# Kernel tuning notes

Hardware: AMD Instinct MI355X
Metric: run time of the kernel (lower is better)

Reference implementation:

```python
import jax, jax.numpy as jnp
import numpy as np

R_SPHERE = 1.0   # conf['object_bounding_sphere']
N_STEPS = 64     # conf['n_steps']
N_IMPORT = 32    # forward default num_samples
VARI = 0.3       # forward default vari -> inv_s = exp(3)


def sdf_fn(pts):
    # analytic stand-in for implicit_network(x, expression)[..., 0]: sphere of radius 0.5
    return jnp.linalg.norm(pts, axis=-1) - 0.5


def sample_pdf(bins, weights, n_samples):
    # deterministic (det=True) CDF inversion, faithful to sample_pdf()
    weights = weights + 1e-8
    pdf = weights / jnp.sum(weights, -1, keepdims=True)
    cdf = jnp.cumsum(pdf, -1)
    cdf = jnp.concatenate([jnp.zeros_like(cdf[..., :1]), cdf], -1)  # [R, n]
    u = jnp.linspace(0.5 / n_samples, 1.0 - 0.5 / n_samples, n_samples, dtype=bins.dtype)
    u = jnp.broadcast_to(u, cdf.shape[:-1] + (n_samples,))          # [R, ns]
    inds = jax.vmap(lambda c, uu: jnp.searchsorted(c, uu, side='right'))(cdf, u)
    below = jnp.maximum(inds - 1, 0)
    above = jnp.minimum(inds, cdf.shape[-1] - 1)
    cdf_b = jnp.take_along_axis(cdf, below, -1)
    cdf_a = jnp.take_along_axis(cdf, above, -1)
    bins_b = jnp.take_along_axis(bins, below, -1)
    bins_a = jnp.take_along_axis(bins, above, -1)
    denom = cdf_a - cdf_b
    denom = jnp.where(denom < 1e-8, jnp.ones_like(denom), denom)
    t = (u - cdf_b) / denom
    return bins_b + t * (bins_a - bins_b)


def setup_inputs() -> dict:
    key = jax.random.key(0)
    k1, k2 = jax.random.split(key)
    rd = jax.random.normal(k1, (1, 262144, 3), dtype=jnp.float32)
    rd = rd / jnp.linalg.norm(rd, axis=-1, keepdims=True)  # unit ray directions
    cam_loc = jnp.array([[0.0, 0.0, 2.5]], dtype=jnp.float32)  # outside bounding sphere
    t_rand = jax.random.uniform(k2, (262144, N_STEPS), dtype=jnp.float32)
    return {"ray_dirs": rd, "cam_loc": cam_loc, "t_rand": t_rand}


def reference(ray_dirs, cam_loc, t_rand):
    b, p, _ = ray_dirs.shape
    # --- get_sphere_intersection ---
    ray_cam_dot = jnp.einsum('bpd,bd->bp', ray_dirs, cam_loc)              # [b,p]
    under = ray_cam_dot ** 2 - (jnp.sum(cam_loc ** 2, -1, keepdims=True) - R_SPHERE ** 2)
    under = under.reshape(-1)
    mask = under > 0
    sq = jnp.sqrt(jnp.where(mask, under, 0.0))
    si = sq[:, None] * jnp.array([-1.0, 1.0], dtype=ray_dirs.dtype) - ray_cam_dot.reshape(-1)[:, None]
    n_hit = jnp.maximum(jnp.sum(mask), 1)
    mean_si = jnp.sum(jnp.where(mask[:, None], si, 0.0), 0) / n_hit
    si = jnp.where(mask[:, None], si, mean_si[None, :])
    si = jnp.clip(si, 0.0, None)                                           # [b*p, 2]
    min_d, max_d = si[:, 0], si[:, 1]
    # --- eval_sdf_inside_sphere: stratified uniform samples (mask_intersect == all ones) ---
    steps = jnp.linspace(0.0, 1.0, N_STEPS, dtype=ray_dirs.dtype)[None, :]
    steps = steps * (max_d - min_d)[:, None] + min_d[:, None]
    sample_dist = ((max_d - min_d) / N_STEPS)[:, None]
    steps = steps + (t_rand - 0.5) * sample_dist                           # [R, n]
    origins = jnp.broadcast_to(cam_loc[:, None, :], (b, p, 3)).reshape(-1, 3)
    dirs = ray_dirs.reshape(-1, 3)
    pts = origins[:, None, :] + steps[..., None] * dirs[:, None, :]        # [R, n, 3]
    sdf = sdf_fn(pts)                                                      # [R, n]
    # --- NeuS alpha / weights ---
    inv_s = jnp.exp(jnp.asarray(VARI, ray_dirs.dtype) * 10.0)
    prev_cdf = jax.nn.sigmoid(sdf[:, :-1] * inv_s)
    next_cdf = jax.nn.sigmoid(sdf[:, 1:] * inv_s)
    alpha = jnp.clip((prev_cdf - next_cdf + 1e-8) / (prev_cdf + 1e-8), 0.0, 1.0)
    trans = jnp.cumprod(jnp.concatenate([jnp.ones((alpha.shape[0], 1), alpha.dtype),
                                         1.0 - alpha + 1e-7], -1), -1)[:, :-1]
    weights = alpha * trans                                                # [R, n-1]
    # --- up_sample: PDF importance resampling (searchsorted + gather) ---
    z_samples = sample_pdf(steps, weights, N_IMPORT)                       # [R, ns]
    new_samples = origins[:, None, :] + z_samples[..., None] * dirs[:, None, :]  # [R, ns, 3]
    return new_samples, z_samples, weights
```

## Files before the change

kernel.cpp:

```cpp
#include <hip/hip_runtime.h>


static constexpr int NSTEPS = 64;
static constexpr int NIMP   = 32;

template<int CTRL, int RM>
__device__ __forceinline__ float upd_dpp_f(float old, float src){
  return __int_as_float(__builtin_amdgcn_update_dpp(
      __float_as_int(old), __float_as_int(src), CTRL, RM, 0xF, false));
}

__device__ __forceinline__ float mul_scan64(float x){
  x *= upd_dpp_f<0x111,0xF>(1.0f, x);
  x *= upd_dpp_f<0x112,0xF>(1.0f, x);
  x *= upd_dpp_f<0x114,0xF>(1.0f, x);
  x *= upd_dpp_f<0x118,0xF>(1.0f, x);
  x *= upd_dpp_f<0x142,0xa>(1.0f, x);
  x *= upd_dpp_f<0x143,0xc>(1.0f, x);
  return x;
}
__device__ __forceinline__ float add_scan64(float x){
  x += upd_dpp_f<0x111,0xF>(0.0f, x);
  x += upd_dpp_f<0x112,0xF>(0.0f, x);
  x += upd_dpp_f<0x114,0xF>(0.0f, x);
  x += upd_dpp_f<0x118,0xF>(0.0f, x);
  x += upd_dpp_f<0x142,0xa>(0.0f, x);
  x += upd_dpp_f<0x143,0xc>(0.0f, x);
  return x;
}

__global__ __launch_bounds__(256) void si_partial_kernel(
    const float* __restrict__ rd, const float* __restrict__ cam,
    float* __restrict__ partial, int P)
{
  float cx = cam[0], cy = cam[1], cz = cam[2];
  float c2m = cx*cx + cy*cy + cz*cz - 1.0f;
  float s0 = 0.f, s1 = 0.f, cnt = 0.f;
  int stride = gridDim.x * blockDim.x;
  for (int p = blockIdx.x * blockDim.x + threadIdx.x; p < P; p += stride){
    float dx = rd[3*p+0], dy = rd[3*p+1], dz = rd[3*p+2];
    float rcd = dx*cx + dy*cy + dz*cz;
    float under = rcd*rcd - c2m;
    if (under > 0.f){
      float sq = sqrtf(under);
      s0 += -sq - rcd; s1 += sq - rcd; cnt += 1.f;
    }
  }
  #pragma unroll
  for (int off = 32; off > 0; off >>= 1){
    s0  += __shfl_down(s0,  off, 64);
    s1  += __shfl_down(s1,  off, 64);
    cnt += __shfl_down(cnt, off, 64);
  }
  __shared__ float sh[3][4];
  int w = threadIdx.x >> 6;
  if ((threadIdx.x & 63) == 0){ sh[0][w] = s0; sh[1][w] = s1; sh[2][w] = cnt; }
  __syncthreads();
  if (threadIdx.x == 0){
    partial[blockIdx.x*3+0] = sh[0][0]+sh[0][1]+sh[0][2]+sh[0][3];
    partial[blockIdx.x*3+1] = sh[1][0]+sh[1][1]+sh[1][2]+sh[1][3];
    partial[blockIdx.x*3+2] = sh[2][0]+sh[2][1]+sh[2][2]+sh[2][3];
  }
}

__global__ __launch_bounds__(256) void si_final_kernel(
    const float* __restrict__ partial, float* __restrict__ ws, int nblk)
{
  float s0 = 0.f, s1 = 0.f, cnt = 0.f;
  for (int b = threadIdx.x; b < nblk; b += 256){
    s0 += partial[3*b+0]; s1 += partial[3*b+1]; cnt += partial[3*b+2];
  }
  #pragma unroll
  for (int off = 32; off > 0; off >>= 1){
    s0  += __shfl_down(s0,  off, 64);
    s1  += __shfl_down(s1,  off, 64);
    cnt += __shfl_down(cnt, off, 64);
  }
  __shared__ float sh[3][4];
  int w = threadIdx.x >> 6;
  if ((threadIdx.x & 63) == 0){ sh[0][w] = s0; sh[1][w] = s1; sh[2][w] = cnt; }
  __syncthreads();
  if (threadIdx.x == 0){
    ws[0] = sh[0][0]+sh[0][1]+sh[0][2]+sh[0][3];
    ws[1] = sh[1][0]+sh[1][1]+sh[1][2]+sh[1][3];
    ws[2] = sh[2][0]+sh[2][1]+sh[2][2]+sh[2][3];
  }
}

__global__ __launch_bounds__(256) void render_wave_kernel(
    const float* __restrict__ rd, const float* __restrict__ cam,
    const float* __restrict__ tr, const float* __restrict__ ws,
    float* __restrict__ out, int P)
{
  const int lane = threadIdx.x & 63;
  const int wid  = (int)((blockIdx.x * blockDim.x + threadIdx.x) >> 6);
  const int nw   = (int)((gridDim.x * blockDim.x) >> 6);

  const float cx = cam[0], cy = cam[1], cz = cam[2];
  const float c2m = cx*cx + cy*cy + cz*cz - 1.0f;
  const float nh = fmaxf(ws[2], 1.0f);
  const float m0 = ws[0] / nh, m1 = ws[1] / nh;

  const float inv_s = 20.085536923187668f;
  const float jf = (float)lane * (1.0f/63.0f);
  const float u  = (float)(2*lane + 1) * (1.0f/64.0f);

  const int e2 = 64 + lane;
  const int q1 = lane / 3, r1 = lane - 3*q1;
  const int q2 = e2  / 3, r2 = e2  - 3*q2;

  for (int p = wid; p < P; p += nw){
    float dx = rd[3*p+0], dy = rd[3*p+1], dz = rd[3*p+2];
    float rcd = dx*cx + dy*cy + dz*cz;
    float under = rcd*rcd - c2m;
    float si0, si1;
    if (under > 0.f){
      float sq = sqrtf(under);
      si0 = -sq - rcd; si1 = sq - rcd;
    } else {
      si0 = m0; si1 = m1;
    }
    float min_d = fmaxf(si0, 0.f), max_d = fmaxf(si1, 0.f);
    float range = max_d - min_d;
    float sdist = range * (1.0f/64.0f);

    float t = tr[(size_t)p*64 + lane];
    float s = fmaf(range, jf, min_d) + (t - 0.5f) * sdist;
    float px = fmaf(s,dx,cx), py = fmaf(s,dy,cy), pz = fmaf(s,dz,cz);
    float c  = 1.0f / (1.0f + __expf(-(sqrtf(px*px+py*py+pz*pz) - 0.5f) * inv_s));

    float cnx = upd_dpp_f<0x130,0xF>(c, c);
    float a = (c - cnx + 1e-8f) / (c + 1e-8f);
    a = fminf(fmaxf(a, 0.f), 1.0f);

    float f = (lane < 63) ? (1.0f - a + 1e-7f) : 1.0f;
    float incl = mul_scan64(f);
    float trans = upd_dpp_f<0x138,0xF>(1.0f, incl);

    float w = a * trans;
    if (lane < 63) out[(size_t)P*128 + (size_t)p*63 + lane] = w;

    float wp = (lane < 63) ? (w + 1e-8f) : 0.0f;
    float D = add_scan64(wp);
    float Tp = __shfl(D, 62, 64);
    float invT = 1.0f / Tp;
    D *= invT;
    if (lane == 63) D = 2.0f;

    int js = 0;
    #pragma unroll
    for (int r = 32; r >= 1; r >>= 1){
      float v = __shfl(D, js + r - 1, 64);
      if (v <= u) js += r;
    }
    float Db = (js > 0) ? __shfl(D, js - 1, 64) : 0.0f;
    float Da = __shfl(D, js, 64);
    float sb = __shfl(s, js, 64);
    float sa = __shfl(s, js + 1, 64);
    float den = Da - Db;
    if (den < 1e-8f) den = 1.0f;
    float tq = (u - Db) / den;
    float z  = fmaf(tq, sa - sb, sb);
    if (lane < 32) out[(size_t)P*96 + (size_t)p*32 + lane] = z;

    float z1 = __shfl(z, q1, 64);
    float dd1 = (r1 == 0) ? dx : ((r1 == 1) ? dy : dz);
    float cc1 = (r1 == 0) ? cx : ((r1 == 1) ? cy : cz);
    out[(size_t)p*96 + lane] = fmaf(z1, dd1, cc1);
    if (lane < 32){
      float z2 = __shfl(z, q2, 64);
      float dd2 = (r2 == 0) ? dx : ((r2 == 1) ? dy : dz);
      float cc2 = (r2 == 0) ? cx : ((r2 == 1) ? cy : cz);
      out[(size_t)p*96 + e2] = fmaf(z2, dd2, cc2);
    }
  }
}

extern "C" void kernel_launch(void* const* d_in, const int* in_sizes, int n_in,
                              void* d_out, int out_size, void* d_ws, size_t ws_size,
                              hipStream_t stream) {
  const float* rd  = (const float*)d_in[0];
  const float* cam = (const float*)d_in[1];
  const float* tr  = (const float*)d_in[2];
  float* out = (float*)d_out;
  float* ws  = (float*)d_ws;
  const int P = in_sizes[0] / 3;

  const int RBLK = 256;
  si_partial_kernel<<<RBLK, 256, 0, stream>>>(rd, cam, ws + 8, P);
  si_final_kernel<<<1, 256, 0, stream>>>(ws + 8, ws, RBLK);
  render_wave_kernel<<<2048, 256, 0, stream>>>(rd, cam, tr, ws, out, P);
}
```

Measured before the change: 303.9 us.

## Replace wave binary search with per-lane scatter inversion and prefetch next ray

Drops the shuffle-based binary search over the CDF. Instead, each lane works out which of the 32 deterministic u samples fall in its own CDF interval, interpolates them, and writes them into a per-wave LDS buffer. The gather for the 3D sample outputs then reads from LDS instead of using cross-lane shuffles. The ray direction and t_rand for the next iteration are loaded ahead of time to hide global-load latency. The cost is a divergent per-lane loop, LDS traffic, and extra live registers for the prefetched values.

```diff
diff --git a/kernel.cpp b/kernel.cpp
--- a/kernel.cpp
+++ b/kernel.cpp
@@ -8,6 +8,10 @@
 __device__ __forceinline__ float upd_dpp_f(float old, float src){
   return __int_as_float(__builtin_amdgcn_update_dpp(
       __float_as_int(old), __float_as_int(src), CTRL, RM, 0xF, false));
+}
+template<int CTRL, int RM>
+__device__ __forceinline__ int upd_dpp_i(int old, int src){
+  return __builtin_amdgcn_update_dpp(old, src, CTRL, RM, 0xF, false);
 }
 
 __device__ __forceinline__ float mul_scan64(float x){
@@ -92,7 +96,9 @@
     const float* __restrict__ tr, const float* __restrict__ ws,
     float* __restrict__ out, int P)
 {
+  __shared__ float zb[4][32];
   const int lane = threadIdx.x & 63;
+  const int wv   = threadIdx.x >> 6;
   const int wid  = (int)((blockIdx.x * blockDim.x + threadIdx.x) >> 6);
   const int nw   = (int)((gridDim.x * blockDim.x) >> 6);
 
@@ -103,14 +109,28 @@
 
   const float inv_s = 20.085536923187668f;
   const float jf = (float)lane * (1.0f/63.0f);
-  const float u  = (float)(2*lane + 1) * (1.0f/64.0f);
 
   const int e2 = 64 + lane;
   const int q1 = lane / 3, r1 = lane - 3*q1;
   const int q2 = e2  / 3, r2 = e2  - 3*q2;
 
+  float* __restrict__ wbase = out + (size_t)P*128;
+  float* __restrict__ zbase = out + (size_t)P*96;
+
+  if (wid >= P) return;
+
+  float dx = rd[3*wid+0], dy = rd[3*wid+1], dz = rd[3*wid+2];
+  float t  = tr[(size_t)wid*64 + lane];
+
   for (int p = wid; p < P; p += nw){
-    float dx = rd[3*p+0], dy = rd[3*p+1], dz = rd[3*p+2];
+    const int pn = p + nw;
+    const bool hasn = pn < P;
+    float dxn = 0.f, dyn = 0.f, dzn = 0.f, tn = 0.f;
+    if (hasn){
+      dxn = rd[3*pn+0]; dyn = rd[3*pn+1]; dzn = rd[3*pn+2];
+      tn  = tr[(size_t)pn*64 + lane];
+    }
+
     float rcd = dx*cx + dy*cy + dz*cz;
     float under = rcd*rcd - c2m;
     float si0, si1;
@@ -124,7 +144,6 @@
     float range = max_d - min_d;
     float sdist = range * (1.0f/64.0f);
 
-    float t = tr[(size_t)p*64 + lane];
     float s = fmaf(range, jf, min_d) + (t - 0.5f) * sdist;
     float px = fmaf(s,dx,cx), py = fmaf(s,dy,cy), pz = fmaf(s,dz,cz);
     float c  = 1.0f / (1.0f + __expf(-(sqrtf(px*px+py*py+pz*pz) - 0.5f) * inv_s));
@@ -138,41 +157,42 @@
     float trans = upd_dpp_f<0x138,0xF>(1.0f, incl);
 
     float w = a * trans;
-    if (lane < 63) out[(size_t)P*128 + (size_t)p*63 + lane] = w;
+    if (lane < 63) wbase[(size_t)p*63 + lane] = w;
 
     float wp = (lane < 63) ? (w + 1e-8f) : 0.0f;
     float D = add_scan64(wp);
-    float Tp = __shfl(D, 62, 64);
-    float invT = 1.0f / Tp;
-    D *= invT;
-    if (lane == 63) D = 2.0f;
-
-    int js = 0;
-    #pragma unroll
-    for (int r = 32; r >= 1; r >>= 1){
-      float v = __shfl(D, js + r - 1, 64);
-      if (v <= u) js += r;
-    }
-    float Db = (js > 0) ? __shfl(D, js - 1, 64) : 0.0f;
-    float Da = __shfl(D, js, 64);
-    float sb = __shfl(s, js, 64);
-    float sa = __shfl(s, js + 1, 64);
-    float den = Da - Db;
+    float Tp = __int_as_float(
+        __builtin_amdgcn_readlane(__float_as_int(D), 62));
+    D *= (1.0f / Tp);
+
+    float Dm1 = upd_dpp_f<0x138,0xF>(0.0f, D);
+    float s1l = upd_dpp_f<0x130,0xF>(s, s);
+    int h = (int)ceilf(fmaf(64.0f, D, -1.0f) * 0.5f);
+    h = max(0, min(32, h));
+    int hm1 = upd_dpp_i<0x138,0xF>(0, h);
+    float den = D - Dm1;
     if (den < 1e-8f) den = 1.0f;
-    float tq = (u - Db) / den;
-    float z  = fmaf(tq, sa - sb, sb);
-    if (lane < 32) out[(size_t)P*96 + (size_t)p*32 + lane] = z;
-
-    float z1 = __shfl(z, q1, 64);
+    float rden = 1.0f / den;
+    for (int i = hm1; i < h; ++i){
+      float u_i = (float)(2*i + 1) * (1.0f/64.0f);
+      float tq = (u_i - Dm1) * rden;
+      zb[wv][i] = fmaf(tq, s1l - s, s);
+    }
+    float z  = zb[wv][lane & 31];
+    float z1 = zb[wv][q1];
+    float z2 = zb[wv][q2];
+    if (lane < 32) zbase[(size_t)p*32 + lane] = z;
+
     float dd1 = (r1 == 0) ? dx : ((r1 == 1) ? dy : dz);
     float cc1 = (r1 == 0) ? cx : ((r1 == 1) ? cy : cz);
     out[(size_t)p*96 + lane] = fmaf(z1, dd1, cc1);
     if (lane < 32){
-      float z2 = __shfl(z, q2, 64);
       float dd2 = (r2 == 0) ? dx : ((r2 == 1) ? dy : dz);
       float cc2 = (r2 == 0) ? cx : ((r2 == 1) ? cy : cz);
       out[(size_t)p*96 + e2] = fmaf(z2, dd2, cc2);
     }
+
+    dx = dxn; dy = dyn; dz = dzn; t = tn;
   }
 }
 
```

Result: slower. 316.3 us (+4.1%).
